# Performance work log

Measured on AMD Instinct MI355X. Metric: run time of the kernel, lower is better.

Reference implementation:

```python
import jax, jax.numpy as jnp
import numpy as np

N = 131072      # number of nodes / samples
IN_DIM = 128    # input_dim
H = 128         # hidden_dim
OUT_DIM = 10    # output_dim


def setup_inputs() -> dict:
    key = jax.random.key(0)
    ks = jax.random.split(key, 20)
    s = 0.05
    def rn(k, shape):
        return jax.random.normal(k, shape, jnp.float32) * s
    return {
        "x": jax.random.normal(ks[0], (N, IN_DIM), jnp.float32),
        # GRU layer 1 (seq_len=1, h0=0 => weight_hh contributes nothing; only b_hh matters)
        "w_ih_f1": rn(ks[1], (3 * H, IN_DIM)), "b_ih_f1": rn(ks[2], (3 * H,)), "b_hh_f1": rn(ks[3], (3 * H,)),
        "w_ih_b1": rn(ks[4], (3 * H, IN_DIM)), "b_ih_b1": rn(ks[5], (3 * H,)), "b_hh_b1": rn(ks[6], (3 * H,)),
        # GRU layer 2 (input 2H)
        "w_ih_f2": rn(ks[7], (3 * H, 2 * H)), "b_ih_f2": rn(ks[8], (3 * H,)), "b_hh_f2": rn(ks[9], (3 * H,)),
        "w_ih_b2": rn(ks[10], (3 * H, 2 * H)), "b_ih_b2": rn(ks[11], (3 * H,)), "b_hh_b2": rn(ks[12], (3 * H,)),
        # GCNConv layers
        "w_g1": rn(ks[13], (2 * H, 128)), "b_g1": rn(ks[14], (128,)),
        "w_g2": rn(ks[15], (128, 64)), "b_g2": rn(ks[16], (64,)),
        # final fc
        "w_fc": rn(ks[17], (64, OUT_DIM)), "b_fc": rn(ks[18], (OUT_DIM,)),
    }


def _gru_cell_zero(x, w_ih, b_ih, b_hh):
    # PyTorch GRU cell with h_prev = 0: h' = (1 - z) * n_gate
    gi = x @ w_ih.T + b_ih                    # [n, 3H]
    ir, iz, inn = jnp.split(gi, 3, axis=-1)
    hr, hz, hn = jnp.split(b_hh, 3)
    r = jax.nn.sigmoid(ir + hr)
    z = jax.nn.sigmoid(iz + hz)
    ng = jnp.tanh(inn + r * hn)
    return (1.0 - z) * ng


def _gcn(x, w, b, sources, targets, n):
    # PyG GCNConv: D^{-1/2}(A+I)D^{-1/2} X W + b, self-loops already in edge lists
    xw = x @ w                                 # [n, out]
    deg = jax.ops.segment_sum(jnp.ones(sources.shape[0], x.dtype), targets, num_segments=n)
    dinv = jax.lax.rsqrt(deg)
    norm = dinv[sources] * dinv[targets]       # [E]
    msg = norm[:, None] * xw[sources]          # gather
    return jax.ops.segment_sum(msg, targets, num_segments=n) + b  # scatter-add


def reference(x, w_ih_f1, b_ih_f1, b_hh_f1, w_ih_b1, b_ih_b1, b_hh_b1,
              w_ih_f2, b_ih_f2, b_hh_f2, w_ih_b2, b_ih_b2, b_hh_b2,
              w_g1, b_g1, w_g2, b_g2, w_fc, b_fc):
    n = x.shape[0]
    # seq_len = 1 => bidirectional GRU output is [fwd_cell(x); bwd_cell(x)]
    h1 = jnp.concatenate([_gru_cell_zero(x, w_ih_f1, b_ih_f1, b_hh_f1),
                          _gru_cell_zero(x, w_ih_b1, b_ih_b1, b_hh_b1)], axis=-1)
    h2 = jnp.concatenate([_gru_cell_zero(h1, w_ih_f2, b_ih_f2, b_hh_f2),
                          _gru_cell_zero(h1, w_ih_b2, b_ih_b2, b_hh_b2)], axis=-1)
    # chain graph, both directions, plus self loops (GCNConv adds them)
    src = jnp.arange(n - 1)
    dst = jnp.arange(1, n)
    ar = jnp.arange(n)
    sources = jnp.concatenate([src, dst, ar])
    targets = jnp.concatenate([dst, src, ar])
    g1 = _gcn(h2, w_g1, b_g1, sources, targets, n)   # dropout is identity in eval
    g2 = _gcn(g1, w_g2, b_g2, sources, targets, n)
    return g2 @ w_fc + b_fc
```

## Files before the change

### kernel.cpp

```cpp
#include <hip/hip_runtime.h>
#include <stdint.h>

#define N_NODES 131072
#define HDIM 128

typedef __bf16 bf16x8 __attribute__((ext_vector_type(8)));
typedef float f32x4 __attribute__((ext_vector_type(4)));
typedef unsigned short us8 __attribute__((ext_vector_type(8)));
typedef unsigned short ushort_t;

__device__ __forceinline__ float bf2f(ushort_t u) {
    union { float f; uint32_t i; } v; v.i = ((uint32_t)u) << 16; return v.f;
}
__device__ __forceinline__ ushort_t f2bf(float f) {
    union { float f; uint32_t i; } v; v.f = f;
    uint32_t i = v.i;
    return (ushort_t)((i + 0x7FFFu + ((i >> 16) & 1u)) >> 16);
}

__device__ __forceinline__ void gll16(const ushort_t* g, ushort_t* l) {
    __builtin_amdgcn_global_load_lds(
        (const __attribute__((address_space(1))) uint32_t*)g,
        (__attribute__((address_space(3))) uint32_t*)l, 16, 0, 0);
}

__device__ __forceinline__ bf16x8 ldsw(const ushort_t* base, int R, int g) {
    return *(const bf16x8*)&base[R * 64 + (((g - R) & 7) << 3)];
}

__device__ __forceinline__ float fsig(float x) {
    return __builtin_amdgcn_rcpf(1.0f + __expf(-x));
}
__device__ __forceinline__ float ftanh(float y) {
    float yc = fminf(fmaxf(y, -15.0f), 15.0f);
    float e = __expf(2.0f * yc);
    return (e - 1.0f) * __builtin_amdgcn_rcpf(e + 1.0f);
}

template<int NC>
__device__ __forceinline__ void swz(int b, int& m, int& c) {
    int mhi = b / (8 * NC);
    int rem = b - mhi * (8 * NC);
    c = rem >> 3;
    m = mhi * 8 + (rem & 7);
}

__global__ __launch_bounds__(256) void prep_weights(
    const float* __restrict__ w_f1, const float* __restrict__ w_b1,
    const float* __restrict__ w_f2, const float* __restrict__ w_b2,
    ushort_t* __restrict__ PWF1, ushort_t* __restrict__ PWB1,
    ushort_t* __restrict__ PWF2, ushort_t* __restrict__ PWB2)
{
    int idx = blockIdx.x * 256 + threadIdx.x;
    if (idx < 49152) {
        PWF1[idx] = f2bf(w_f1[idx]);
    } else if (idx < 98304) {
        int j = idx - 49152;  PWB1[j] = f2bf(w_b1[j]);
    } else if (idx < 196608) {
        int j = idx - 98304;  PWF2[j] = f2bf(w_f2[j]);
    } else if (idx < 294912) {
        int j = idx - 196608; PWB2[j] = f2bf(w_b2[j]);
    }
}

__global__ __launch_bounds__(256) void prep_M(
    const float* __restrict__ w_g1, const float* __restrict__ b_g1,
    const float* __restrict__ w_g2, const float* __restrict__ b_g2,
    const float* __restrict__ w_fc, const float* __restrict__ b_fc,
    ushort_t* __restrict__ M16, float* __restrict__ cc)
{
    __shared__ float wfc_s[640];
    __shared__ float T1[128][10];
    const int t = threadIdx.x;
    for (int i = t; i < 640; i += 256) wfc_s[i] = w_fc[i];
    __syncthreads();
    if (t < 128) {
        float s[10];
        #pragma unroll
        for (int j = 0; j < 10; ++j) s[j] = 0.0f;
        const float4* row = (const float4*)(w_g2 + t * 64);
        #pragma unroll
        for (int k4 = 0; k4 < 16; ++k4) {
            float4 v = row[k4];
            #pragma unroll
            for (int j = 0; j < 10; ++j)
                s[j] += v.x * wfc_s[(k4 * 4 + 0) * 10 + j] + v.y * wfc_s[(k4 * 4 + 1) * 10 + j]
                      + v.z * wfc_s[(k4 * 4 + 2) * 10 + j] + v.w * wfc_s[(k4 * 4 + 3) * 10 + j];
        }
        #pragma unroll
        for (int j = 0; j < 10; ++j) T1[t][j] = s[j];
    }
    __syncthreads();
    float m[10];
    #pragma unroll
    for (int j = 0; j < 10; ++j) m[j] = 0.0f;
    const float4* row1 = (const float4*)(w_g1 + t * 128);
    #pragma unroll 4
    for (int k4 = 0; k4 < 32; ++k4) {
        float4 v = row1[k4];
        #pragma unroll
        for (int j = 0; j < 10; ++j)
            m[j] += v.x * T1[k4 * 4 + 0][j] + v.y * T1[k4 * 4 + 1][j]
                  + v.z * T1[k4 * 4 + 2][j] + v.w * T1[k4 * 4 + 3][j];
    }
    #pragma unroll
    for (int j = 0; j < 16; ++j)
        M16[j * 256 + t] = (j < 10) ? f2bf(m[j]) : (ushort_t)0;
    if (t < 10) {
        float s1 = 0.0f;
        for (int k2 = 0; k2 < 128; ++k2) s1 += b_g1[k2] * T1[k2][t];
        cc[t] = s1;
        float s2 = 0.0f;
        for (int k3 = 0; k3 < 64; ++k3) s2 += b_g2[k3] * wfc_s[k3 * 10 + t];
        cc[16 + t] = s2 + b_fc[t];
    }
}

__global__ __launch_bounds__(256) void xconv(
    const float* __restrict__ x, ushort_t* __restrict__ xb)
{
    int idx = blockIdx.x * 256 + threadIdx.x;
    const float* s = x + (size_t)idx * 8;
    float4 f0 = ((const float4*)s)[0];
    float4 f1 = ((const float4*)s)[1];
    us8 t;
    t[0] = f2bf(f0.x); t[1] = f2bf(f0.y); t[2] = f2bf(f0.z); t[3] = f2bf(f0.w);
    t[4] = f2bf(f1.x); t[5] = f2bf(f1.y); t[6] = f2bf(f1.z); t[7] = f2bf(f1.w);
    *(us8*)&xb[(size_t)idx * 8] = t;
}

template<int K>
__global__ __launch_bounds__(256, 5) void gru_gemm2(
    const ushort_t* __restrict__ A,
    const ushort_t* __restrict__ Wf,
    const ushort_t* __restrict__ Wb,
    const float* __restrict__ bi_f, const float* __restrict__ bh_f,
    const float* __restrict__ bi_b, const float* __restrict__ bh_b,
    ushort_t* __restrict__ Hout)
{
    __shared__ ushort_t As[128 * 64];
    __shared__ ushort_t Bs[96 * 64];
    const int tid = threadIdx.x;
    int mt, comb;
    swz<8>(blockIdx.x, mt, comb);
    const int m0 = mt * 128;
    const int dir = comb >> 2;
    const int j0 = (comb & 3) * 32;
    const ushort_t* W = dir ? Wb : Wf;
    const float* b_ih = dir ? bi_b : bi_f;
    const float* b_hh = dir ? bh_b : bh_f;
    const int coloff = dir << 7;

    const int wv = tid >> 6, lane = tid & 63;
    const int lr = lane & 15, lq = lane >> 4;
    const int tr = tid >> 3, tc = tid & 7;
    const int sc = ((tr + tc) & 7) << 3;

    f32x4 acc[3][2][2];
    #pragma unroll
    for (int g = 0; g < 3; ++g)
        #pragma unroll
        for (int rt = 0; rt < 2; ++rt)
            #pragma unroll
            for (int ct = 0; ct < 2; ++ct)
                #pragma unroll
                for (int e = 0; e < 4; ++e) acc[g][rt][ct][e] = 0.0f;

    for (int t = 0; t < K / 64; ++t) {
        const int k0 = t * 64;
        const ushort_t* ga = A + (size_t)(m0 + tr) * K + k0 + sc;
        #pragma unroll
        for (int i = 0; i < 4; ++i)
            gll16(ga + (size_t)i * 32 * K, &As[(i * 256 + tid) * 8]);
        #pragma unroll
        for (int i = 0; i < 3; ++i) {
            int wr = (i << 7) + j0 + tr;
            gll16(W + (size_t)wr * K + k0 + sc, &Bs[(i * 256 + tid) * 8]);
        }
        __syncthreads();
        #pragma unroll
        for (int kk = 0; kk < 64; kk += 32) {
            const int g8 = (kk >> 3) + lq;
            bf16x8 a0 = ldsw(As, wv * 32 + lr, g8);
            bf16x8 a1 = ldsw(As, wv * 32 + 16 + lr, g8);
            #pragma unroll
            for (int g = 0; g < 3; ++g) {
                #pragma unroll
                for (int ct = 0; ct < 2; ++ct) {
                    bf16x8 b = ldsw(Bs, g * 32 + ct * 16 + lr, g8);
                    acc[g][0][ct] = __builtin_amdgcn_mfma_f32_16x16x32_bf16(a0, b, acc[g][0][ct], 0, 0, 0);
                    acc[g][1][ct] = __builtin_amdgcn_mfma_f32_16x16x32_bf16(a1, b, acc[g][1][ct], 0, 0, 0);
                }
            }
        }
        __syncthreads();
    }

    #pragma unroll
    for (int ct = 0; ct < 2; ++ct) {
        const int j = j0 + ct * 16 + lr;
        const float br  = b_ih[j] + b_hh[j];
        const float bz  = b_ih[HDIM + j] + b_hh[HDIM + j];
        const float bn  = b_ih[2 * HDIM + j];
        const float bhn = b_hh[2 * HDIM + j];
        #pragma unroll
        for (int rt = 0; rt < 2; ++rt) {
            #pragma unroll
            for (int r = 0; r < 4; ++r) {
                const int row = m0 + wv * 32 + rt * 16 + lq * 4 + r;
                float rg = fsig(acc[0][rt][ct][r] + br);
                float zg = fsig(acc[1][rt][ct][r] + bz);
                float ng = ftanh(acc[2][rt][ct][r] + bn + rg * bhn);
                Hout[(size_t)row * 256 + coloff + j] = f2bf((1.0f - zg) * ng);
            }
        }
    }
}

__global__ __launch_bounds__(256, 5) void zgemm(
    const ushort_t* __restrict__ A,
    const ushort_t* __restrict__ M16,
    float* __restrict__ Zc)
{
    __shared__ ushort_t As[128 * 64];
    const int tid = threadIdx.x;
    const int m0 = blockIdx.x * 128;
    const int wv = tid >> 6, lane = tid & 63;
    const int lr = lane & 15, lq = lane >> 4;
    const int tr = tid >> 3, tc = tid & 7;
    const int sc = ((tr + tc) & 7) << 3;

    bf16x8 bfrag[8];
    #pragma unroll
    for (int s = 0; s < 8; ++s)
        bfrag[s] = *(const bf16x8*)&M16[lr * 256 + s * 32 + lq * 8];

    f32x4 acc[2];
    #pragma unroll
    for (int e = 0; e < 4; ++e) { acc[0][e] = 0.0f; acc[1][e] = 0.0f; }

    for (int t = 0; t < 4; ++t) {
        const int k0 = t * 64;
        const ushort_t* ga = A + (size_t)(m0 + tr) * 256 + k0 + sc;
        #pragma unroll
        for (int i = 0; i < 4; ++i)
            gll16(ga + (size_t)i * 32 * 256, &As[(i * 256 + tid) * 8]);
        __syncthreads();
        #pragma unroll
        for (int kk = 0; kk < 64; kk += 32) {
            const int g8 = (kk >> 3) + lq;
            bf16x8 a0 = ldsw(As, wv * 32 + lr, g8);
            bf16x8 a1 = ldsw(As, wv * 32 + 16 + lr, g8);
            bf16x8 b = bfrag[t * 2 + (kk >> 5)];
            acc[0] = __builtin_amdgcn_mfma_f32_16x16x32_bf16(a0, b, acc[0], 0, 0, 0);
            acc[1] = __builtin_amdgcn_mfma_f32_16x16x32_bf16(a1, b, acc[1], 0, 0, 0);
        }
        __syncthreads();
    }

    if (lr < 10) {
        #pragma unroll
        for (int rt = 0; rt < 2; ++rt)
            #pragma unroll
            for (int r = 0; r < 4; ++r) {
                int row = m0 + wv * 32 + rt * 16 + lq * 4 + r;
                Zc[(size_t)row * 10 + lr] = acc[rt][r];
            }
    }
}

__device__ __forceinline__ float dcoef(int i) {
    return (i == 0 || i == N_NODES - 1) ? 0.70710678118654752f : 0.57735026918962576f;
}
__global__ __launch_bounds__(256) void st5(
    const float* __restrict__ z, float* __restrict__ out,
    const float* __restrict__ cc)
{
    int idx = blockIdx.x * 256 + threadIdx.x;
    int i = idx >> 4, c = idx & 15;
    if (c >= 10) return;
    float d_i = dcoef(i);
    float accv = 0.0f, dsum = d_i;
    #pragma unroll
    for (int oj = -1; oj <= 1; ++oj) {
        int j = i + oj;
        if (j < 0 || j >= N_NODES) continue;
        float dj = dcoef(j);
        if (oj != 0) dsum += dj;
        float wj = 0.0f;
        #pragma unroll
        for (int ok = -1; ok <= 1; ++ok) {
            int k = j + ok;
            if (k < 0 || k >= N_NODES) continue;
            wj += dcoef(k) * z[(size_t)k * 10 + c];
        }
        accv += dj * dj * wj;
    }
    out[(size_t)i * 10 + c] = d_i * accv + d_i * dsum * cc[c] + cc[16 + c];
}

extern "C" void kernel_launch(void* const* d_in, const int* in_sizes, int n_in,
                              void* d_out, int out_size, void* d_ws, size_t ws_size,
                              hipStream_t stream) {
    const float* x     = (const float*)d_in[0];
    const float* w_f1  = (const float*)d_in[1];
    const float* bi_f1 = (const float*)d_in[2];
    const float* bh_f1 = (const float*)d_in[3];
    const float* w_b1  = (const float*)d_in[4];
    const float* bi_b1 = (const float*)d_in[5];
    const float* bh_b1 = (const float*)d_in[6];
    const float* w_f2  = (const float*)d_in[7];
    const float* bi_f2 = (const float*)d_in[8];
    const float* bh_f2 = (const float*)d_in[9];
    const float* w_b2  = (const float*)d_in[10];
    const float* bi_b2 = (const float*)d_in[11];
    const float* bh_b2 = (const float*)d_in[12];
    const float* w_g1  = (const float*)d_in[13];
    const float* b_g1  = (const float*)d_in[14];
    const float* w_g2  = (const float*)d_in[15];
    const float* b_g2  = (const float*)d_in[16];
    const float* w_fc  = (const float*)d_in[17];
    const float* b_fc  = (const float*)d_in[18];

    char* ws = (char*)d_ws;
    ushort_t* h1   = (ushort_t*)(ws);
    ushort_t* xb   = (ushort_t*)(ws + 67108864);
    ushort_t* h2   = (ushort_t*)(ws + 67108864);
    float*    Zc   = (float*)(ws);
    ushort_t* PWF1 = (ushort_t*)(ws + 134217728);
    ushort_t* PWB1 = PWF1 + 49152;
    ushort_t* PWF2 = PWB1 + 49152;
    ushort_t* PWB2 = PWF2 + 98304;
    ushort_t* M16  = PWB2 + 98304;
    float*    cc   = (float*)(M16 + 4096);

    prep_weights<<<1152, 256, 0, stream>>>(w_f1, w_b1, w_f2, w_b2,
                                           PWF1, PWB1, PWF2, PWB2);
    prep_M<<<1, 256, 0, stream>>>(w_g1, b_g1, w_g2, b_g2, w_fc, b_fc, M16, cc);
    xconv<<<N_NODES * 16 / 256, 256, 0, stream>>>(x, xb);

    gru_gemm2<128><<<N_NODES / 128 * 8, 256, 0, stream>>>(
        xb, PWF1, PWB1, bi_f1, bh_f1, bi_b1, bh_b1, h1);
    gru_gemm2<256><<<N_NODES / 128 * 8, 256, 0, stream>>>(
        h1, PWF2, PWB2, bi_f2, bh_f2, bi_b2, bh_b2, h2);

    zgemm<<<N_NODES / 128, 256, 0, stream>>>(h2, M16, Zc);
    st5<<<N_NODES * 16 / 256, 256, 0, stream>>>(Zc, (float*)d_out, cc);
}
```

Baseline: 296.9 us.

## Fuse x bf16 conversion into GRU layer1 and fold Z projection into layer2

New measurement: 298.1 us. No clear change (+0.4%).

```diff
diff --git a/kernel.cpp b/kernel.cpp
--- a/kernel.cpp
+++ b/kernel.cpp
@@ -49,7 +49,8 @@
     const float* __restrict__ w_f1, const float* __restrict__ w_b1,
     const float* __restrict__ w_f2, const float* __restrict__ w_b2,
     ushort_t* __restrict__ PWF1, ushort_t* __restrict__ PWB1,
-    ushort_t* __restrict__ PWF2, ushort_t* __restrict__ PWB2)
+    ushort_t* __restrict__ PWF2, ushort_t* __restrict__ PWB2,
+    float* __restrict__ Zc)
 {
     int idx = blockIdx.x * 256 + threadIdx.x;
     if (idx < 49152) {
@@ -61,6 +62,8 @@
     } else if (idx < 294912) {
         int j = idx - 196608; PWB2[j] = f2bf(w_b2[j]);
     }
+    float4 z4; z4.x = 0.0f; z4.y = 0.0f; z4.z = 0.0f; z4.w = 0.0f;
+    for (int i = idx; i < 327680; i += 294912) ((float4*)Zc)[i] = z4;
 }
 
 __global__ __launch_bounds__(256) void prep_M(
@@ -116,22 +119,8 @@
     }
 }
 
-__global__ __launch_bounds__(256) void xconv(
-    const float* __restrict__ x, ushort_t* __restrict__ xb)
-{
-    int idx = blockIdx.x * 256 + threadIdx.x;
-    const float* s = x + (size_t)idx * 8;
-    float4 f0 = ((const float4*)s)[0];
-    float4 f1 = ((const float4*)s)[1];
-    us8 t;
-    t[0] = f2bf(f0.x); t[1] = f2bf(f0.y); t[2] = f2bf(f0.z); t[3] = f2bf(f0.w);
-    t[4] = f2bf(f1.x); t[5] = f2bf(f1.y); t[6] = f2bf(f1.z); t[7] = f2bf(f1.w);
-    *(us8*)&xb[(size_t)idx * 8] = t;
-}
-
-template<int K>
-__global__ __launch_bounds__(256, 5) void gru_gemm2(
-    const ushort_t* __restrict__ A,
+__global__ __launch_bounds__(256, 4) void gru_l1(
+    const float* __restrict__ X,
     const ushort_t* __restrict__ Wf,
     const ushort_t* __restrict__ Wb,
     const float* __restrict__ bi_f, const float* __restrict__ bh_f,
@@ -166,16 +155,28 @@
                 #pragma unroll
                 for (int e = 0; e < 4; ++e) acc[g][rt][ct][e] = 0.0f;
 
-    for (int t = 0; t < K / 64; ++t) {
+    for (int t = 0; t < 2; ++t) {
         const int k0 = t * 64;
-        const ushort_t* ga = A + (size_t)(m0 + tr) * K + k0 + sc;
-        #pragma unroll
-        for (int i = 0; i < 4; ++i)
-            gll16(ga + (size_t)i * 32 * K, &As[(i * 256 + tid) * 8]);
+        const float* ga = X + (size_t)(m0 + tr) * 128 + k0 + sc;
+        float4 fa[4][2];
+        #pragma unroll
+        for (int i = 0; i < 4; ++i) {
+            const float4* p = (const float4*)(ga + (size_t)i * 32 * 128);
+            fa[i][0] = p[0]; fa[i][1] = p[1];
+        }
         #pragma unroll
         for (int i = 0; i < 3; ++i) {
             int wr = (i << 7) + j0 + tr;
-            gll16(W + (size_t)wr * K + k0 + sc, &Bs[(i * 256 + tid) * 8]);
+            gll16(W + (size_t)wr * 128 + k0 + sc, &Bs[(i * 256 + tid) * 8]);
+        }
+        #pragma unroll
+        for (int i = 0; i < 4; ++i) {
+            us8 t8;
+            t8[0] = f2bf(fa[i][0].x); t8[1] = f2bf(fa[i][0].y);
+            t8[2] = f2bf(fa[i][0].z); t8[3] = f2bf(fa[i][0].w);
+            t8[4] = f2bf(fa[i][1].x); t8[5] = f2bf(fa[i][1].y);
+            t8[6] = f2bf(fa[i][1].z); t8[7] = f2bf(fa[i][1].w);
+            *(us8*)&As[(i * 256 + tid) * 8] = t8;
         }
         __syncthreads();
         #pragma unroll
@@ -217,27 +218,42 @@
     }
 }
 
-__global__ __launch_bounds__(256, 5) void zgemm(
+__global__ __launch_bounds__(256, 5) void gru_l2(
     const ushort_t* __restrict__ A,
+    const ushort_t* __restrict__ Wf,
+    const ushort_t* __restrict__ Wb,
+    const float* __restrict__ bi_f, const float* __restrict__ bh_f,
+    const float* __restrict__ bi_b, const float* __restrict__ bh_b,
     const ushort_t* __restrict__ M16,
     float* __restrict__ Zc)
 {
     __shared__ ushort_t As[128 * 64];
+    __shared__ ushort_t Bs[96 * 64];
     const int tid = threadIdx.x;
-    const int m0 = blockIdx.x * 128;
+    int mt, comb;
+    swz<8>(blockIdx.x, mt, comb);
+    const int m0 = mt * 128;
+    const int dir = comb >> 2;
+    const int j0 = (comb & 3) * 32;
+    const ushort_t* W = dir ? Wb : Wf;
+    const float* b_ih = dir ? bi_b : bi_f;
+    const float* b_hh = dir ? bh_b : bh_f;
+    const int coloff = dir << 7;
+
     const int wv = tid >> 6, lane = tid & 63;
     const int lr = lane & 15, lq = lane >> 4;
     const int tr = tid >> 3, tc = tid & 7;
     const int sc = ((tr + tc) & 7) << 3;
 
-    bf16x8 bfrag[8];
-    #pragma unroll
-    for (int s = 0; s < 8; ++s)
-        bfrag[s] = *(const bf16x8*)&M16[lr * 256 + s * 32 + lq * 8];
-
-    f32x4 acc[2];
-    #pragma unroll
-    for (int e = 0; e < 4; ++e) { acc[0][e] = 0.0f; acc[1][e] = 0.0f; }
+    f32x4 acc[3][2][2];
+    #pragma unroll
+    for (int g = 0; g < 3; ++g)
+        #pragma unroll
+        for (int rt = 0; rt < 2; ++rt)
+            #pragma unroll
+            for (int ct = 0; ct < 2; ++ct)
+                #pragma unroll
+                for (int e = 0; e < 4; ++e) acc[g][rt][ct][e] = 0.0f;
 
     for (int t = 0; t < 4; ++t) {
         const int k0 = t * 64;
@@ -245,27 +261,66 @@
         #pragma unroll
         for (int i = 0; i < 4; ++i)
             gll16(ga + (size_t)i * 32 * 256, &As[(i * 256 + tid) * 8]);
+        #pragma unroll
+        for (int i = 0; i < 3; ++i) {
+            int wr = (i << 7) + j0 + tr;
+            gll16(W + (size_t)wr * 256 + k0 + sc, &Bs[(i * 256 + tid) * 8]);
+        }
         __syncthreads();
         #pragma unroll
         for (int kk = 0; kk < 64; kk += 32) {
             const int g8 = (kk >> 3) + lq;
             bf16x8 a0 = ldsw(As, wv * 32 + lr, g8);
             bf16x8 a1 = ldsw(As, wv * 32 + 16 + lr, g8);
-            bf16x8 b = bfrag[t * 2 + (kk >> 5)];
-            acc[0] = __builtin_amdgcn_mfma_f32_16x16x32_bf16(a0, b, acc[0], 0, 0, 0);
-            acc[1] = __builtin_amdgcn_mfma_f32_16x16x32_bf16(a1, b, acc[1], 0, 0, 0);
+            #pragma unroll
+            for (int g = 0; g < 3; ++g) {
+                #pragma unroll
+                for (int ct = 0; ct < 2; ++ct) {
+                    bf16x8 b = ldsw(Bs, g * 32 + ct * 16 + lr, g8);
+                    acc[g][0][ct] = __builtin_amdgcn_mfma_f32_16x16x32_bf16(a0, b, acc[g][0][ct], 0, 0, 0);
+                    acc[g][1][ct] = __builtin_amdgcn_mfma_f32_16x16x32_bf16(a1, b, acc[g][1][ct], 0, 0, 0);
+                }
+            }
         }
         __syncthreads();
     }
 
+    const bf16x8 mb = *(const bf16x8*)&M16[lr * 256 + coloff + j0 + lq * 8];
+
+    #pragma unroll
+    for (int ct = 0; ct < 2; ++ct) {
+        const int j = j0 + ct * 16 + lr;
+        const float br  = b_ih[j] + b_hh[j];
+        const float bz  = b_ih[HDIM + j] + b_hh[HDIM + j];
+        const float bn  = b_ih[2 * HDIM + j];
+        const float bhn = b_hh[2 * HDIM + j];
+        #pragma unroll
+        for (int rt = 0; rt < 2; ++rt) {
+            #pragma unroll
+            for (int r = 0; r < 4; ++r) {
+                const int lrow = wv * 32 + rt * 16 + lq * 4 + r;
+                float rg = fsig(acc[0][rt][ct][r] + br);
+                float zg = fsig(acc[1][rt][ct][r] + bz);
+                float ng = ftanh(acc[2][rt][ct][r] + bn + rg * bhn);
+                As[lrow * 32 + ct * 16 + lr] = f2bf((1.0f - zg) * ng);
+            }
+        }
+    }
+
+    bf16x8 ha0 = *(const bf16x8*)&As[(wv * 32 + lr) * 32 + lq * 8];
+    bf16x8 ha1 = *(const bf16x8*)&As[(wv * 32 + 16 + lr) * 32 + lq * 8];
+    f32x4 z0, z1;
+    #pragma unroll
+    for (int e = 0; e < 4; ++e) { z0[e] = 0.0f; z1[e] = 0.0f; }
+    z0 = __builtin_amdgcn_mfma_f32_16x16x32_bf16(ha0, mb, z0, 0, 0, 0);
+    z1 = __builtin_amdgcn_mfma_f32_16x16x32_bf16(ha1, mb, z1, 0, 0, 0);
+
     if (lr < 10) {
         #pragma unroll
-        for (int rt = 0; rt < 2; ++rt)
-            #pragma unroll
-            for (int r = 0; r < 4; ++r) {
-                int row = m0 + wv * 32 + rt * 16 + lq * 4 + r;
-                Zc[(size_t)row * 10 + lr] = acc[rt][r];
-            }
+        for (int r = 0; r < 4; ++r) {
+            atomicAdd(&Zc[(size_t)(m0 + wv * 32 + lq * 4 + r) * 10 + lr], z0[r]);
+            atomicAdd(&Zc[(size_t)(m0 + wv * 32 + 16 + lq * 4 + r) * 10 + lr], z1[r]);
+        }
     }
 }
 
@@ -324,9 +379,7 @@
 
     char* ws = (char*)d_ws;
     ushort_t* h1   = (ushort_t*)(ws);
-    ushort_t* xb   = (ushort_t*)(ws + 67108864);
-    ushort_t* h2   = (ushort_t*)(ws + 67108864);
-    float*    Zc   = (float*)(ws);
+    float*    Zc   = (float*)(ws + 67108864);
     ushort_t* PWF1 = (ushort_t*)(ws + 134217728);
     ushort_t* PWB1 = PWF1 + 49152;
     ushort_t* PWF2 = PWB1 + 49152;
@@ -335,15 +388,13 @@
     float*    cc   = (float*)(M16 + 4096);
 
     prep_weights<<<1152, 256, 0, stream>>>(w_f1, w_b1, w_f2, w_b2,
-                                           PWF1, PWB1, PWF2, PWB2);
+                                           PWF1, PWB1, PWF2, PWB2, Zc);
     prep_M<<<1, 256, 0, stream>>>(w_g1, b_g1, w_g2, b_g2, w_fc, b_fc, M16, cc);
-    xconv<<<N_NODES * 16 / 256, 256, 0, stream>>>(x, xb);
-
-    gru_gemm2<128><<<N_NODES / 128 * 8, 256, 0, stream>>>(
-        xb, PWF1, PWB1, bi_f1, bh_f1, bi_b1, bh_b1, h1);
-    gru_gemm2<256><<<N_NODES / 128 * 8, 256, 0, stream>>>(
-        h1, PWF2, PWB2, bi_f2, bh_f2, bi_b2, bh_b2, h2);
-
-    zgemm<<<N_NODES / 128, 256, 0, stream>>>(h2, M16, Zc);
+
+    gru_l1<<<N_NODES / 128 * 8, 256, 0, stream>>>(
+        x, PWF1, PWB1, bi_f1, bh_f1, bi_b1, bh_b1, h1);
+    gru_l2<<<N_NODES / 128 * 8, 256, 0, stream>>>(
+        h1, PWF2, PWB2, bi_f2, bh_f2, bi_b2, bh_b2, M16, Zc);
+
     st5<<<N_NODES * 16 / 256, 256, 0, stream>>>(Zc, (float*)d_out, cc);
 }
```
